# Performance work log

Hardware: AMD Instinct MI355X
Metric: run time of the kernel (lower is better)

The kernel has to match this reference:

```python
import jax, jax.numpy as jnp
import numpy as np

NUM_HEADS = 16
ROPE_THETA = 1000.0


def _rope(x, cos, sin):
    # x: [B, H, T, d_k]; cos/sin: [T, d_k//2]
    xp = x.reshape(x.shape[:-1] + (x.shape[-1] // 2, 2))
    xe, xo = xp[..., 0], xp[..., 1]
    c = cos[None, None, :, :]
    s = sin[None, None, :, :]
    re = xe * c - xo * s
    ro = xe * s + xo * c
    return jnp.stack((re, ro), axis=-1).reshape(x.shape)


def setup_inputs() -> dict:
    key = jax.random.key(0)
    ks = jax.random.split(key, 5)
    B, T, D = 2, 2048, 1024
    std = 2.0 / (D + D)
    return {
        "x": jax.random.normal(ks[0], (B, T, D), dtype=jnp.float32),
        "wq": jax.random.normal(ks[1], (D, D), dtype=jnp.float32) * std,
        "wk": jax.random.normal(ks[2], (D, D), dtype=jnp.float32) * std,
        "wv": jax.random.normal(ks[3], (D, D), dtype=jnp.float32) * std,
        "wo": jax.random.normal(ks[4], (D, D), dtype=jnp.float32) * std,
    }


def reference(x, wq, wk, wv, wo):
    B, T, D = x.shape
    H = NUM_HEADS
    dk = D // H

    def proj(w):
        # Linear stores weight as [out, in]: '... in, out in -> ... out'
        y = jnp.einsum('btd,ed->bte', x, w)
        return y.reshape(B, T, H, dk).transpose(0, 2, 1, 3)  # [B,H,T,dk]

    q = proj(wq)
    k = proj(wk)
    v = proj(wv)

    # RoPE tables
    pos = jnp.arange(T, dtype=jnp.float32)[:, None]
    kidx = jnp.arange(dk // 2, dtype=jnp.float32)
    inv_freq = ROPE_THETA ** (-2.0 * kidx / dk)
    ang = pos * inv_freq[None, :]
    cos, sin = jnp.cos(ang), jnp.sin(ang)

    q = _rope(q, cos, sin)
    k = _rope(k, cos, sin)

    scores = jnp.einsum('bhnd,bhmd->bhnm', q, k) / jnp.sqrt(jnp.asarray(dk, x.dtype))
    causal = jnp.tril(jnp.ones((T, T), dtype=bool))
    scores = jnp.where(causal[None, None], scores, -jnp.inf)
    attn = jax.nn.softmax(scores, axis=-1)
    head = jnp.einsum('bhnm,bhmd->bhnd', attn, v)  # [B,H,T,dk]

    concat = head.transpose(0, 2, 1, 3).reshape(B, T, D)
    return jnp.einsum('btd,ed->bte', concat, wo)
```

## Files before the change

### kernel.cpp

```cpp
#include <hip/hip_runtime.h>
#include <hip/hip_bf16.h>

typedef __hip_bfloat16 bf16;
typedef __attribute__((ext_vector_type(8))) short bf16x8;
typedef __attribute__((ext_vector_type(4))) float f32x4;

#define T_SEQ 2048
#define NHEADS 16
#define DK 64
#define DMODEL 1024

__device__ inline void load_lds16(const void* g, void* l) {
    __builtin_amdgcn_global_load_lds((const __attribute__((address_space(1))) void*)g,
                                     (__attribute__((address_space(3))) void*)l, 16, 0, 0);
}

__global__ void cvt_all(const float* __restrict__ x,  const float* __restrict__ wq,
                        const float* __restrict__ wk, const float* __restrict__ wv,
                        const float* __restrict__ wo, bf16* __restrict__ xb,
                        bf16* __restrict__ wqkvb, bf16* __restrict__ wob) {
    int i = blockIdx.x * blockDim.x + threadIdx.x;
    const float* src; bf16* dst; int off;
    if (i < (1 << 20)) { src = x; dst = xb; off = i; }
    else {
        int j = i - (1 << 20);
        int seg = j >> 18; off = j & ((1 << 18) - 1);
        src = (seg == 0) ? wq : (seg == 1) ? wk : (seg == 2) ? wv : wo;
        dst = (seg < 3) ? (wqkvb + ((size_t)seg << 20)) : wob;
    }
    float4 f = ((const float4*)src)[off];
    ushort4 o;
    o.x = __bfloat16_as_ushort(__float2bfloat16(f.x));
    o.y = __bfloat16_as_ushort(__float2bfloat16(f.y));
    o.z = __bfloat16_as_ushort(__float2bfloat16(f.z));
    o.w = __bfloat16_as_ushort(__float2bfloat16(f.w));
    ((ushort4*)dst)[off] = o;
}

__global__ __launch_bounds__(256) void gemm_qkv_rope(const bf16* __restrict__ A,
                                                     const bf16* __restrict__ B,
                                                     bf16* __restrict__ qb,
                                                     bf16* __restrict__ kb,
                                                     bf16* __restrict__ vt) {
    const int K = 1024, N = 3072;
    __shared__ bf16 As[128 * 32];
    __shared__ bf16 Bs[128 * 32];
    const int tid  = threadIdx.x;
    const int lane = tid & 63;
    const int wave = tid >> 6;
    const int l16  = lane & 15;
    const int quad = lane >> 4;
    const int wy = wave >> 1, wx = wave & 1;
    const int brow = blockIdx.y * 128;
    const int bcol = blockIdx.x * 128;

    f32x4 acc[4][4] = {};

    for (int k0 = 0; k0 < K; k0 += 32) {
#pragma unroll
        for (int i = 0; i < 2; ++i) {
            int j   = tid + 256 * i;
            int row = j >> 2;
            int cc  = j & 3;
            load_lds16(A + (size_t)(brow + row) * K + k0 + cc * 8, (char*)As + j * 16);
            load_lds16(B + (size_t)(bcol + row) * K + k0 + cc * 8, (char*)Bs + j * 16);
        }
        __syncthreads();
        bf16x8 af[4], bq[4];
#pragma unroll
        for (int i = 0; i < 4; ++i)
            af[i] = *(const bf16x8*)(As + (wy * 64 + i * 16 + l16) * 32 + quad * 8);
#pragma unroll
        for (int j = 0; j < 4; ++j)
            bq[j] = *(const bf16x8*)(Bs + (wx * 64 + j * 16 + l16) * 32 + quad * 8);
#pragma unroll
        for (int i = 0; i < 4; ++i)
#pragma unroll
            for (int j = 0; j < 4; ++j)
                acc[i][j] = __builtin_amdgcn_mfma_f32_16x16x32_bf16(af[i], bq[j], acc[i][j], 0, 0, 0);
        __syncthreads();
    }
    const int seg = bcol >> 10;
    const int hh  = ((bcol & 1023) >> 6) + wx;
    if (seg < 2) {
        bf16* dst = seg ? kb : qb;
        const float osc = seg ? 1.0f : 0.18033688011112042f;
#pragma unroll
        for (int j = 0; j < 4; ++j) {
            const int d = j * 16 + l16;
            const float inv = exp2f(-0.31143075889f * (float)(d >> 1));
#pragma unroll
            for (int i = 0; i < 4; ++i)
#pragma unroll
                for (int r = 0; r < 4; ++r) {
                    int row = brow + wy * 64 + i * 16 + quad * 4 + r;
                    int t = row & (T_SEQ - 1), bi = row >> 11;
                    float s, c;
                    __sincosf((float)t * inv, &s, &c);
                    float v = acc[i][j][r];
                    float p = __shfl_xor(v, 1);
                    float res = (l16 & 1) ? fmaf(p, s, v * c) : fmaf(-p, s, v * c);
                    dst[((size_t)(bi * NHEADS + hh) * T_SEQ + t) * DK + d] =
                        __float2bfloat16(res * osc);
                }
        }
    } else {
#pragma unroll
        for (int j = 0; j < 4; ++j) {
            const int d = j * 16 + l16;
#pragma unroll
            for (int i = 0; i < 4; ++i)
#pragma unroll
                for (int r = 0; r < 4; ++r) {
                    int row = brow + wy * 64 + i * 16 + quad * 4 + r;
                    int t = row & (T_SEQ - 1), bi = row >> 11;
                    vt[((size_t)(bi * NHEADS + hh) * DK + d) * T_SEQ + t] =
                        __float2bfloat16(acc[i][j][r]);
                }
        }
    }
}

__global__ __launch_bounds__(256) void gemm_bt(const bf16* __restrict__ A,
                                               const bf16* __restrict__ B,
                                               float* __restrict__ C,
                                               int M, int N, int K) {
    __shared__ bf16 As[128 * 32];
    __shared__ bf16 Bs[128 * 32];
    const int tid  = threadIdx.x;
    const int lane = tid & 63;
    const int wave = tid >> 6;
    const int l16  = lane & 15;
    const int quad = lane >> 4;
    const int wy = wave >> 1, wx = wave & 1;
    const int brow = blockIdx.y * 128;
    const int bcol = blockIdx.x * 128;

    f32x4 acc[4][4] = {};

    for (int k0 = 0; k0 < K; k0 += 32) {
#pragma unroll
        for (int i = 0; i < 2; ++i) {
            int j   = tid + 256 * i;
            int row = j >> 2;
            int cc  = j & 3;
            load_lds16(A + (size_t)(brow + row) * K + k0 + cc * 8, (char*)As + j * 16);
            load_lds16(B + (size_t)(bcol + row) * K + k0 + cc * 8, (char*)Bs + j * 16);
        }
        __syncthreads();
        bf16x8 af[4], bq[4];
#pragma unroll
        for (int i = 0; i < 4; ++i)
            af[i] = *(const bf16x8*)(As + (wy * 64 + i * 16 + l16) * 32 + quad * 8);
#pragma unroll
        for (int j = 0; j < 4; ++j)
            bq[j] = *(const bf16x8*)(Bs + (wx * 64 + j * 16 + l16) * 32 + quad * 8);
#pragma unroll
        for (int i = 0; i < 4; ++i)
#pragma unroll
            for (int j = 0; j < 4; ++j)
                acc[i][j] = __builtin_amdgcn_mfma_f32_16x16x32_bf16(af[i], bq[j], acc[i][j], 0, 0, 0);
        __syncthreads();
    }
#pragma unroll
    for (int i = 0; i < 4; ++i)
#pragma unroll
        for (int j = 0; j < 4; ++j)
#pragma unroll
            for (int r = 0; r < 4; ++r) {
                int row = brow + wy * 64 + i * 16 + quad * 4 + r;
                int col = bcol + wx * 64 + j * 16 + l16;
                C[(size_t)row * N + col] = acc[i][j][r];
            }
}

#define PSTRIDE 72
__constant__ unsigned char c_sched[24] = {
    28, 61, 57, 58, 24, 53, 49, 20,
    62, 54, 50, 41, 42, 16, 45, 46,
     0,  4,  8, 12, 33, 37, 34, 38};

__global__ __launch_bounds__(256) void attn_kernel(const bf16* __restrict__ qb,
                                                   const bf16* __restrict__ kb,
                                                   const bf16* __restrict__ vt,
                                                   float* __restrict__ Oacc,
                                                   float* __restrict__ Lacc,
                                                   bf16* __restrict__ conc) {
    __shared__ bf16 Ks[2][64 * 64];
    __shared__ bf16 Vs[2][64 * 64];
    __shared__ bf16 Pl[4][2][16 * PSTRIDE];
    const int bh = blockIdx.y;
    const int b = bh >> 4, h = bh & 15;

    const int e    = c_sched[blockIdx.x];
    const int tile = e >> 2, mode = e & 3;
    const int it0  = (mode == 2) ? tile + 1 : 0;
    const int it1  = (mode == 1) ? tile : 2 * tile + 1;
    const bool partial = (mode != 0);
    const int qbase = tile << 7;

    const int tid = threadIdx.x;
    const int lane = tid & 63, wave = tid >> 6;
    const int l16 = lane & 15, quad = lane >> 4;
    const int qr0 = qbase + wave * 16;
    const int qr1 = qr0 + 64;

    const bf16* Qp = qb + (size_t)bh * T_SEQ * DK;
    const bf16* Kp = kb + (size_t)bh * T_SEQ * DK;
    const bf16* Vp = vt + (size_t)bh * DK * T_SEQ;
    bf16* Pw0 = &Pl[wave][0][0];
    bf16* Pw1 = &Pl[wave][1][0];

    bf16x8 qf[2][2];
#pragma unroll
    for (int s = 0; s < 2; ++s) {
        qf[0][s] = *(const bf16x8*)(Qp + (size_t)(qr0 + l16) * DK + s * 32 + quad * 8);
        qf[1][s] = *(const bf16x8*)(Qp + (size_t)(qr1 + l16) * DK + s * 32 + quad * 8);
    }

    auto stage = [&](int bb, int k0) {
        int j = tid;
#pragma unroll
        for (int i = 0; i < 2; ++i, j += 256) {
            int row = j >> 3, cbl = (j & 7) ^ ((j >> 3) & 7);
            load_lds16(Kp + (size_t)(k0 + row) * DK + cbl * 8, (char*)Ks[bb] + j * 16);
        }
        j = tid;
#pragma unroll
        for (int i = 0; i < 2; ++i, j += 256) {
            int row = j >> 3, cbl = (j & 7) ^ ((j >> 3) & 7);
            load_lds16(Vp + (size_t)row * T_SEQ + k0 + cbl * 8, (char*)Vs[bb] + j * 16);
        }
    };

    f32x4 o0[4] = {}, o1[4] = {};
    float l0 = 0.0f, l1 = 0.0f;
    const int sw0 = (quad ^ (l16 & 7)) * 8;
    const int sw1 = ((4 + quad) ^ (l16 & 7)) * 8;

    int cur = 0;
    stage(0, it0 * 64);
    for (int it = it0; it <= it1; ++it) {
        __syncthreads();
        if (it < it1) stage(cur ^ 1, (it + 1) * 64);

        const int k0 = it * 64;
        const bool skip0 = (k0 > qr0 + 15);
        const bool diag0 = (k0 + 63 > qr0) && !skip0;
        const bool diag1 = (k0 + 63 > qr1);

        f32x4 s0[4] = {}, s1[4] = {};
#pragma unroll
        for (int nt = 0; nt < 4; ++nt) {
            bf16x8 kf0 = *(const bf16x8*)(Ks[cur] + (nt * 16 + l16) * 64 + sw0);
            bf16x8 kf1 = *(const bf16x8*)(Ks[cur] + (nt * 16 + l16) * 64 + sw1);
            if (!skip0) {
                s0[nt] = __builtin_amdgcn_mfma_f32_16x16x32_bf16(kf0, qf[0][0], s0[nt], 0, 0, 0);
                s0[nt] = __builtin_amdgcn_mfma_f32_16x16x32_bf16(kf1, qf[0][1], s0[nt], 0, 0, 0);
            }
            s1[nt] = __builtin_amdgcn_mfma_f32_16x16x32_bf16(kf0, qf[1][0], s1[nt], 0, 0, 0);
            s1[nt] = __builtin_amdgcn_mfma_f32_16x16x32_bf16(kf1, qf[1][1], s1[nt], 0, 0, 0);
        }
        if (!skip0) {
#pragma unroll
            for (int nt = 0; nt < 4; ++nt) {
                union { bf16 hv[4]; uint2 u; } pk;
#pragma unroll
                for (int r = 0; r < 4; ++r) {
                    float v = s0[nt][r];
                    if (diag0 && (k0 + nt * 16 + quad * 4 + r > qr0 + l16)) v = -30.0f;
                    float p = exp2f(v);
                    l0 += p;
                    pk.hv[r] = __float2bfloat16(p);
                }
                *(uint2*)(Pw0 + l16 * PSTRIDE + nt * 16 + quad * 4) = pk.u;
            }
        }
#pragma unroll
        for (int nt = 0; nt < 4; ++nt) {
            union { bf16 hv[4]; uint2 u; } pk;
#pragma unroll
            for (int r = 0; r < 4; ++r) {
                float v = s1[nt][r];
                if (diag1 && (k0 + nt * 16 + quad * 4 + r > qr1 + l16)) v = -30.0f;
                float p = exp2f(v);
                l1 += p;
                pk.hv[r] = __float2bfloat16(p);
            }
            *(uint2*)(Pw1 + l16 * PSTRIDE + nt * 16 + quad * 4) = pk.u;
        }
#pragma unroll
        for (int ks = 0; ks < 2; ++ks) {
            const int sw = ks ? sw1 : sw0;
            bf16x8 vf[4];
#pragma unroll
            for (int j = 0; j < 4; ++j)
                vf[j] = *(const bf16x8*)(Vs[cur] + (j * 16 + l16) * 64 + sw);
            if (!skip0) {
                bf16x8 pf0 = *(const bf16x8*)(Pw0 + l16 * PSTRIDE + ks * 32 + quad * 8);
#pragma unroll
                for (int j = 0; j < 4; ++j)
                    o0[j] = __builtin_amdgcn_mfma_f32_16x16x32_bf16(pf0, vf[j], o0[j], 0, 0, 0);
            }
            bf16x8 pf1 = *(const bf16x8*)(Pw1 + l16 * PSTRIDE + ks * 32 + quad * 8);
#pragma unroll
            for (int j = 0; j < 4; ++j)
                o1[j] = __builtin_amdgcn_mfma_f32_16x16x32_bf16(pf1, vf[j], o1[j], 0, 0, 0);
        }
        cur ^= 1;
    }
#pragma unroll
    for (int g = 0; g < 2; ++g) {
        float lt = g ? l1 : l0;
        lt += __shfl_xor(lt, 16);
        lt += __shfl_xor(lt, 32);
        const int qr = g ? qr1 : qr0;
        if (!partial) {
#pragma unroll
            for (int r = 0; r < 4; ++r) {
                float lr = __shfl(lt, quad * 4 + r);
                float inv_l = 1.0f / lr;
                int t = qr + quad * 4 + r;
#pragma unroll
                for (int j = 0; j < 4; ++j) {
                    float ov = g ? o1[j][r] : o0[j][r];
                    conc[((size_t)b * T_SEQ + t) * DMODEL + h * DK + j * 16 + l16] =
                        __float2bfloat16(ov * inv_l);
                }
            }
        } else {
            if (quad == 0)
                atomicAdd(&Lacc[(size_t)bh * 1024 + qr + l16 - 1024], lt);
#pragma unroll
            for (int r = 0; r < 4; ++r) {
                int q = qr + quad * 4 + r;
                float* Ob = Oacc + ((size_t)bh * 1024 + q - 1024) * DK;
#pragma unroll
                for (int j = 0; j < 4; ++j) {
                    float ov = g ? o1[j][r] : o0[j][r];
                    atomicAdd(&Ob[j * 16 + l16], ov);
                }
            }
        }
    }
}

__global__ void attn_finalize(const float* __restrict__ Oacc, const float* __restrict__ Lacc,
                              bf16* __restrict__ conc) {
    int i4 = blockIdx.x * blockDim.x + threadIdx.x;
    if (i4 >= (1 << 19)) return;
    int bhq = i4 >> 4;
    int d4  = i4 & 15;
    int bh = bhq >> 10, q1 = bhq & 1023;
    int b = bh >> 4, h = bh & 15;
    int q = 1024 + q1;
    float inv = 1.0f / Lacc[bhq];
    float4 o4 = ((const float4*)Oacc)[i4];
    ushort4 u;
    u.x = __bfloat16_as_ushort(__float2bfloat16(o4.x * inv));
    u.y = __bfloat16_as_ushort(__float2bfloat16(o4.y * inv));
    u.z = __bfloat16_as_ushort(__float2bfloat16(o4.z * inv));
    u.w = __bfloat16_as_ushort(__float2bfloat16(o4.w * inv));
    *(ushort4*)&conc[((size_t)(b * T_SEQ + q)) * DMODEL + h * DK + d4 * 4] = u;
}

extern "C" void kernel_launch(void* const* d_in, const int* in_sizes, int n_in,
                              void* d_out, int out_size, void* d_ws, size_t ws_size,
                              hipStream_t stream) {
    const float* x  = (const float*)d_in[0];
    const float* wq = (const float*)d_in[1];
    const float* wk = (const float*)d_in[2];
    const float* wv = (const float*)d_in[3];
    const float* wo = (const float*)d_in[4];
    float* out = (float*)d_out;

    char* ws = (char*)d_ws;
    bf16* xb    = (bf16*)(ws);
    bf16* wqkvb = (bf16*)(ws + (8ull << 20));
    bf16* wob   = (bf16*)(ws + (14ull << 20));
    bf16* qb    = (bf16*)(ws + (40ull << 20));
    bf16* kb    = (bf16*)(ws + (48ull << 20));
    bf16* vt    = (bf16*)(ws + (56ull << 20));
    bf16* conc  = (bf16*)(ws + (16ull << 20));
    float* Oacc = (float*)(ws + (24ull << 20));
    float* Lacc = (float*)(ws + (32ull << 20));

    cvt_all<<<8192, 256, 0, stream>>>(x, wq, wk, wv, wo, xb, wqkvb, wob);
    gemm_qkv_rope<<<dim3(24, 32), 256, 0, stream>>>(xb, wqkvb, qb, kb, vt);

    hipMemsetAsync(Oacc, 0, (8ull << 20) + 32 * 1024 * sizeof(float), stream);
    attn_kernel<<<dim3(24, 32), 256, 0, stream>>>(qb, kb, vt, Oacc, Lacc, conc);
    attn_finalize<<<2048, 256, 0, stream>>>(Oacc, Lacc, conc);

    gemm_bt<<<dim3(8, 32), 256, 0, stream>>>(conc, wob, out, 4096, 1024, 1024);
}
```

Measured before the change: 210.2 us.

## Compute softmax row sums via MFMA with ones, share one swizzled P buffer

Drops the scalar per-element running sum of probabilities and the shuffle reductions at the end. Row sums now come from an extra MFMA of the bf16 P tile against a ones vector, so the denominator matches the rounded P values used in the PV product. The two per-wave P staging buffers become one XOR-swizzled 16x64 buffer that is reused for each half, and PV runs right after each half's exponentials. The change also adds s_setprio around the MFMA sections and a launch_bounds occupancy hint of 4. In exchange it spends extra MFMAs and serializes the two halves through the shared P buffer.

```diff
diff --git a/kernel.cpp b/kernel.cpp
--- a/kernel.cpp
+++ b/kernel.cpp
@@ -174,21 +174,20 @@
             }
 }
 
-#define PSTRIDE 72
 __constant__ unsigned char c_sched[24] = {
     28, 61, 57, 58, 24, 53, 49, 20,
     62, 54, 50, 41, 42, 16, 45, 46,
      0,  4,  8, 12, 33, 37, 34, 38};
 
-__global__ __launch_bounds__(256) void attn_kernel(const bf16* __restrict__ qb,
-                                                   const bf16* __restrict__ kb,
-                                                   const bf16* __restrict__ vt,
-                                                   float* __restrict__ Oacc,
-                                                   float* __restrict__ Lacc,
-                                                   bf16* __restrict__ conc) {
+__global__ __launch_bounds__(256, 4) void attn_kernel(const bf16* __restrict__ qb,
+                                                      const bf16* __restrict__ kb,
+                                                      const bf16* __restrict__ vt,
+                                                      float* __restrict__ Oacc,
+                                                      float* __restrict__ Lacc,
+                                                      bf16* __restrict__ conc) {
     __shared__ bf16 Ks[2][64 * 64];
     __shared__ bf16 Vs[2][64 * 64];
-    __shared__ bf16 Pl[4][2][16 * PSTRIDE];
+    __shared__ bf16 Pl[4][16 * 64];
     const int bh = blockIdx.y;
     const int b = bh >> 4, h = bh & 15;
 
@@ -208,8 +207,11 @@
     const bf16* Qp = qb + (size_t)bh * T_SEQ * DK;
     const bf16* Kp = kb + (size_t)bh * T_SEQ * DK;
     const bf16* Vp = vt + (size_t)bh * DK * T_SEQ;
-    bf16* Pw0 = &Pl[wave][0][0];
-    bf16* Pw1 = &Pl[wave][1][0];
+    char* Pw = (char*)&Pl[wave][0];
+
+    const short one_bits = 0x3F80;
+    const bf16x8 ones = {one_bits, one_bits, one_bits, one_bits,
+                         one_bits, one_bits, one_bits, one_bits};
 
     bf16x8 qf[2][2];
 #pragma unroll
@@ -234,9 +236,11 @@
     };
 
     f32x4 o0[4] = {}, o1[4] = {};
-    float l0 = 0.0f, l1 = 0.0f;
+    f32x4 ol0 = {}, ol1 = {};
     const int sw0 = (quad ^ (l16 & 7)) * 8;
     const int sw1 = ((4 + quad) ^ (l16 & 7)) * 8;
+    const int pw_wr_base = l16 * 128 + (quad & 1) * 8;
+    const int pq = quad >> 1, pql = quad & 1;
 
     int cur = 0;
     stage(0, it0 * 64);
@@ -250,6 +254,7 @@
         const bool diag1 = (k0 + 63 > qr1);
 
         f32x4 s0[4] = {}, s1[4] = {};
+        __builtin_amdgcn_s_setprio(1);
 #pragma unroll
         for (int nt = 0; nt < 4; ++nt) {
             bf16x8 kf0 = *(const bf16x8*)(Ks[cur] + (nt * 16 + l16) * 64 + sw0);
@@ -261,6 +266,8 @@
             s1[nt] = __builtin_amdgcn_mfma_f32_16x16x32_bf16(kf0, qf[1][0], s1[nt], 0, 0, 0);
             s1[nt] = __builtin_amdgcn_mfma_f32_16x16x32_bf16(kf1, qf[1][1], s1[nt], 0, 0, 0);
         }
+        __builtin_amdgcn_s_setprio(0);
+
         if (!skip0) {
 #pragma unroll
             for (int nt = 0; nt < 4; ++nt) {
@@ -269,13 +276,25 @@
                 for (int r = 0; r < 4; ++r) {
                     float v = s0[nt][r];
                     if (diag0 && (k0 + nt * 16 + quad * 4 + r > qr0 + l16)) v = -30.0f;
-                    float p = exp2f(v);
-                    l0 += p;
-                    pk.hv[r] = __float2bfloat16(p);
+                    pk.hv[r] = __float2bfloat16(exp2f(v));
                 }
-                *(uint2*)(Pw0 + l16 * PSTRIDE + nt * 16 + quad * 4) = pk.u;
-            }
-        }
+                *(uint2*)(Pw + pw_wr_base + (((nt * 2 + pq) ^ (l16 & 7)) << 4)) = pk.u;
+            }
+            __builtin_amdgcn_s_setprio(1);
+#pragma unroll
+            for (int ks = 0; ks < 2; ++ks) {
+                bf16x8 pf = *(const bf16x8*)(Pw + l16 * 128 + (((ks * 4 + quad) ^ (l16 & 7)) << 4));
+                const int sw = ks ? sw1 : sw0;
+                ol0 = __builtin_amdgcn_mfma_f32_16x16x32_bf16(pf, ones, ol0, 0, 0, 0);
+#pragma unroll
+                for (int j = 0; j < 4; ++j) {
+                    bf16x8 vf = *(const bf16x8*)(Vs[cur] + (j * 16 + l16) * 64 + sw);
+                    o0[j] = __builtin_amdgcn_mfma_f32_16x16x32_bf16(pf, vf, o0[j], 0, 0, 0);
+                }
+            }
+            __builtin_amdgcn_s_setprio(0);
+        }
+
 #pragma unroll
         for (int nt = 0; nt < 4; ++nt) {
             union { bf16 hv[4]; uint2 u; } pk;
@@ -283,63 +302,51 @@
             for (int r = 0; r < 4; ++r) {
                 float v = s1[nt][r];
                 if (diag1 && (k0 + nt * 16 + quad * 4 + r > qr1 + l16)) v = -30.0f;
-                float p = exp2f(v);
-                l1 += p;
-                pk.hv[r] = __float2bfloat16(p);
-            }
-            *(uint2*)(Pw1 + l16 * PSTRIDE + nt * 16 + quad * 4) = pk.u;
-        }
+                pk.hv[r] = __float2bfloat16(exp2f(v));
+            }
+            *(uint2*)(Pw + pw_wr_base + (((nt * 2 + pq) ^ (l16 & 7)) << 4)) = pk.u;
+        }
+        __builtin_amdgcn_s_setprio(1);
 #pragma unroll
         for (int ks = 0; ks < 2; ++ks) {
+            bf16x8 pf = *(const bf16x8*)(Pw + l16 * 128 + (((ks * 4 + quad) ^ (l16 & 7)) << 4));
             const int sw = ks ? sw1 : sw0;
-            bf16x8 vf[4];
-#pragma unroll
-            for (int j = 0; j < 4; ++j)
-                vf[j] = *(const bf16x8*)(Vs[cur] + (j * 16 + l16) * 64 + sw);
-            if (!skip0) {
-                bf16x8 pf0 = *(const bf16x8*)(Pw0 + l16 * PSTRIDE + ks * 32 + quad * 8);
-#pragma unroll
-                for (int j = 0; j < 4; ++j)
-                    o0[j] = __builtin_amdgcn_mfma_f32_16x16x32_bf16(pf0, vf[j], o0[j], 0, 0, 0);
-            }
-            bf16x8 pf1 = *(const bf16x8*)(Pw1 + l16 * PSTRIDE + ks * 32 + quad * 8);
-#pragma unroll
-            for (int j = 0; j < 4; ++j)
-                o1[j] = __builtin_amdgcn_mfma_f32_16x16x32_bf16(pf1, vf[j], o1[j], 0, 0, 0);
-        }
+            ol1 = __builtin_amdgcn_mfma_f32_16x16x32_bf16(pf, ones, ol1, 0, 0, 0);
+#pragma unroll
+            for (int j = 0; j < 4; ++j) {
+                bf16x8 vf = *(const bf16x8*)(Vs[cur] + (j * 16 + l16) * 64 + sw);
+                o1[j] = __builtin_amdgcn_mfma_f32_16x16x32_bf16(pf, vf, o1[j], 0, 0, 0);
+            }
+        }
+        __builtin_amdgcn_s_setprio(0);
         cur ^= 1;
     }
+
 #pragma unroll
     for (int g = 0; g < 2; ++g) {
-        float lt = g ? l1 : l0;
-        lt += __shfl_xor(lt, 16);
-        lt += __shfl_xor(lt, 32);
+        const f32x4* op = g ? o1 : o0;
+        const f32x4 lv = g ? ol1 : ol0;
         const int qr = g ? qr1 : qr0;
         if (!partial) {
 #pragma unroll
             for (int r = 0; r < 4; ++r) {
-                float lr = __shfl(lt, quad * 4 + r);
-                float inv_l = 1.0f / lr;
+                float inv_l = 1.0f / lv[r];
                 int t = qr + quad * 4 + r;
 #pragma unroll
-                for (int j = 0; j < 4; ++j) {
-                    float ov = g ? o1[j][r] : o0[j][r];
+                for (int j = 0; j < 4; ++j)
                     conc[((size_t)b * T_SEQ + t) * DMODEL + h * DK + j * 16 + l16] =
-                        __float2bfloat16(ov * inv_l);
-                }
+                        __float2bfloat16(op[j][r] * inv_l);
             }
         } else {
-            if (quad == 0)
-                atomicAdd(&Lacc[(size_t)bh * 1024 + qr + l16 - 1024], lt);
 #pragma unroll
             for (int r = 0; r < 4; ++r) {
                 int q = qr + quad * 4 + r;
+                if (l16 == 0)
+                    atomicAdd(&Lacc[(size_t)bh * 1024 + q - 1024], lv[r]);
                 float* Ob = Oacc + ((size_t)bh * 1024 + q - 1024) * DK;
 #pragma unroll
-                for (int j = 0; j < 4; ++j) {
-                    float ov = g ? o1[j][r] : o0[j][r];
-                    atomicAdd(&Ob[j * 16 + l16], ov);
-                }
+                for (int j = 0; j < 4; ++j)
+                    atomicAdd(&Ob[j * 16 + l16], op[j][r]);
             }
         }
     }
```

Measured after the change: 209.9 us. Within noise of the previous version (-0.1%).
